# Kernel optimization log

Hardware: AMD Instinct MI355X
Metric: run time of the kernel (lower is better)

Reference implementation:

```python
import jax, jax.numpy as jnp
import numpy as np

MAX_REL_POS = 16  # max_relative_position


def setup_inputs() -> dict:
    key = jax.random.key(0)
    k1, k2, k3 = jax.random.split(key, 3)
    B, H, Lq, Dh = 4, 8, 1024, 64
    L = 1024
    query = jax.random.normal(k1, (B, H, Lq, Dh), dtype=jnp.float32)
    rel_table = jax.random.normal(k2, (2 * MAX_REL_POS + 1, Dh), dtype=jnp.float32)
    time_ids = jnp.sort(jax.random.randint(k3, (B, L), 0, 4096), axis=-1).astype(jnp.int64)
    return {"query": query, "rel_table": rel_table, "time_ids": time_ids, "k_len": 1024}


def reference(query, rel_table, time_ids, k_len):
    # query: (B,H,Lq,Dh), rel_table: (2P+1, Dh), time_ids: (B,L)
    q_len = query.shape[2]
    ts = time_ids[:, :k_len]                       # (B, Lk)
    # relative position: time_k - time_q -> (B, Lq, Lk)
    rel_pos = ts[:, None, :] - ts[:, :q_len, None]
    idx = jnp.clip(rel_pos, -MAX_REL_POS, MAX_REL_POS) + MAX_REL_POS
    rel_emb = rel_table[idx]                       # (B, Lq, Lk, Dh) gather
    # content-to-position scores
    return jnp.einsum("bhqd,bqkd->bhqk", query, rel_emb)
```

## Files before the change

kernel.cpp:

```cpp
#include <hip/hip_runtime.h>

#define MAX_REL 16
#define NTAB    33
#define B       4
#define H       8
#define LQ      1024
#define DH      64
#define KLEN    1024
#define QTILE   16
#define TSTRIDE 68

__global__ __launch_bounds__(256) void fused_pe_kernel(const float* __restrict__ query,
                                                       const float* __restrict__ table,
                                                       const int* __restrict__ time_ids,
                                                       float* __restrict__ out) {
    __shared__ int   ts[KLEN];
    __shared__ float qt[QTILE * DH];
    __shared__ float tb[NTAB * TSTRIDE];
    __shared__ float pr[QTILE * NTAB];

    const int tid  = threadIdx.x;
    const int wave = tid >> 6;
    const int lane = tid & 63;
    const int tile = blockIdx.x;
    const int bh   = tile >> 6;
    const int qt_i = tile & 63;
    const int b    = bh >> 3;
    const int q0   = qt_i * QTILE;
    const int rowbase = bh * LQ + q0;

    ((int4*)ts)[tid] = ((const int4*)(time_ids + b * KLEN))[tid];
    ((float4*)qt)[tid] = ((const float4*)(query + (size_t)rowbase * DH))[tid];
    for (int i = tid; i < NTAB * 16; i += 256) {
        int r = i >> 4, c = i & 15;
        ((float4*)(tb + r * TSTRIDE))[c] = ((const float4*)(table + r * DH))[c];
    }
    __syncthreads();

    const int r0 = wave * 4;
    for (int t = lane; t < 4 * NTAB; t += 64) {
        int r = t / NTAB;
        int j = t - r * NTAB;
        const float4* qv = (const float4*)(qt + (r0 + r) * DH);
        const float4* tv = (const float4*)(tb + j * TSTRIDE);
        float acc = 0.f;
#pragma unroll
        for (int i = 0; i < DH / 4; ++i) {
            float4 a = qv[i];
            float4 w = tv[i];
            acc += a.x * w.x + a.y * w.y + a.z * w.z + a.w * w.w;
        }
        pr[(r0 + r) * NTAB + j] = acc;
    }

    const int4 tk0 = ((const int4*)ts)[0 * 64 + lane];
    const int4 tk1 = ((const int4*)ts)[1 * 64 + lane];
    const int4 tk2 = ((const int4*)ts)[2 * 64 + lane];
    const int4 tk3 = ((const int4*)ts)[3 * 64 + lane];

#pragma unroll
    for (int r = 0; r < 4; ++r) {
        const int row = r0 + r;
        const int tq  = ts[q0 + row];
        const float* prr = pr + row * NTAB;
        float* op = out + (size_t)(rowbase + row) * KLEN + (lane << 2);
#pragma unroll
        for (int c = 0; c < 4; ++c) {
            int4 tk = (c == 0) ? tk0 : (c == 1) ? tk1 : (c == 2) ? tk2 : tk3;
            int i0 = min(max(tk.x - tq, -MAX_REL), MAX_REL) + MAX_REL;
            int i1 = min(max(tk.y - tq, -MAX_REL), MAX_REL) + MAX_REL;
            int i2 = min(max(tk.z - tq, -MAX_REL), MAX_REL) + MAX_REL;
            int i3 = min(max(tk.w - tq, -MAX_REL), MAX_REL) + MAX_REL;
            float4 v = make_float4(prr[i0], prr[i1], prr[i2], prr[i3]);
            *((float4*)(op + c * 256)) = v;
        }
    }
}

extern "C" void kernel_launch(void* const* d_in, const int* in_sizes, int n_in,
                              void* d_out, int out_size, void* d_ws, size_t ws_size,
                              hipStream_t stream) {
    const float* query    = (const float*)d_in[0];
    const float* table    = (const float*)d_in[1];
    const int*   time_ids = (const int*)d_in[2];
    float* out = (float*)d_out;

    fused_pe_kernel<<<B * H * (LQ / QTILE), 256, 0, stream>>>(query, table, time_ids, out);
}
```

Baseline: 146.5 us.

## Compute query-table projection with bf16 MFMA instead of scalar FP32 dot products

Converts the query tile and the relative-position table to bf16 in shared memory, laid out for the matrix cores, and computes the 16x33 projection with mfma_f32_16x16x32_bf16 instructions instead of per-lane FP32 dot products. Each wave computes the full projection redundantly and writes back only its own four rows. This targets the compute phase ahead of the gather/store, but bf16 rounding lowers accuracy. The kernel is likely bound by output writes, so the gain may be small.

```diff
diff --git a/kernel.cpp b/kernel.cpp
--- a/kernel.cpp
+++ b/kernel.cpp
@@ -8,16 +8,25 @@
 #define DH      64
 #define KLEN    1024
 #define QTILE   16
-#define TSTRIDE 68
+#define PRS     48
+
+typedef short s16x8 __attribute__((ext_vector_type(8)));
+typedef float f32x4 __attribute__((ext_vector_type(4)));
+
+static __device__ __forceinline__ short f2bf(float f) {
+    unsigned u = __float_as_uint(f);
+    unsigned r = (u + 0x7FFFu + ((u >> 16) & 1u)) >> 16;
+    return (short)r;
+}
 
 __global__ __launch_bounds__(256) void fused_pe_kernel(const float* __restrict__ query,
                                                        const float* __restrict__ table,
                                                        const int* __restrict__ time_ids,
                                                        float* __restrict__ out) {
     __shared__ int   ts[KLEN];
-    __shared__ float qt[QTILE * DH];
-    __shared__ float tb[NTAB * TSTRIDE];
-    __shared__ float pr[QTILE * NTAB];
+    __shared__ short qth[2 * 64 * 8];
+    __shared__ short tbh[2 * 4 * 48 * 8];
+    __shared__ float pr[QTILE * PRS];
 
     const int tid  = threadIdx.x;
     const int wave = tid >> 6;
@@ -30,27 +39,45 @@
     const int rowbase = bh * LQ + q0;
 
     ((int4*)ts)[tid] = ((const int4*)(time_ids + b * KLEN))[tid];
-    ((float4*)qt)[tid] = ((const float4*)(query + (size_t)rowbase * DH))[tid];
+
+    {
+        float4 v = ((const float4*)(query + (size_t)rowbase * DH))[tid];
+        int m = tid >> 4, c = tid & 15;
+        int kstep = c >> 3, quad = (c >> 1) & 3, jb = (c & 1) << 2;
+        short4 hv = make_short4(f2bf(v.x), f2bf(v.y), f2bf(v.z), f2bf(v.w));
+        *(short4*)(qth + ((kstep * 64 + quad * 16 + m) << 3) + jb) = hv;
+    }
     for (int i = tid; i < NTAB * 16; i += 256) {
-        int r = i >> 4, c = i & 15;
-        ((float4*)(tb + r * TSTRIDE))[c] = ((const float4*)(table + r * DH))[c];
+        int n = i >> 4, c = i & 15;
+        float4 v = ((const float4*)table)[i];
+        int kstep = c >> 3, quad = (c >> 1) & 3, jb = (c & 1) << 2;
+        short4 hv = make_short4(f2bf(v.x), f2bf(v.y), f2bf(v.z), f2bf(v.w));
+        *(short4*)(tbh + (((kstep * 4 + quad) * 48 + n) << 3) + jb) = hv;
     }
     __syncthreads();
 
-    const int r0 = wave * 4;
-    for (int t = lane; t < 4 * NTAB; t += 64) {
-        int r = t / NTAB;
-        int j = t - r * NTAB;
-        const float4* qv = (const float4*)(qt + (r0 + r) * DH);
-        const float4* tv = (const float4*)(tb + j * TSTRIDE);
-        float acc = 0.f;
+    const int quad = lane >> 4;
+    const int nlo  = lane & 15;
+    f32x4 acc0 = {0.f, 0.f, 0.f, 0.f}, acc1 = acc0, acc2 = acc0;
 #pragma unroll
-        for (int i = 0; i < DH / 4; ++i) {
-            float4 a = qv[i];
-            float4 w = tv[i];
-            acc += a.x * w.x + a.y * w.y + a.z * w.z + a.w * w.w;
+    for (int kstep = 0; kstep < 2; ++kstep) {
+        s16x8 a = *(const s16x8*)(qth + ((kstep * 64 + lane) << 3));
+        const short* bbase = tbh + (((kstep * 4 + quad) * 48) << 3);
+        s16x8 b0 = *(const s16x8*)(bbase + (nlo << 3));
+        s16x8 b1 = *(const s16x8*)(bbase + ((nlo + 16) << 3));
+        s16x8 b2 = *(const s16x8*)(bbase + (32 << 3));
+        acc0 = __builtin_amdgcn_mfma_f32_16x16x32_bf16(a, b0, acc0, 0, 0, 0);
+        acc1 = __builtin_amdgcn_mfma_f32_16x16x32_bf16(a, b1, acc1, 0, 0, 0);
+        acc2 = __builtin_amdgcn_mfma_f32_16x16x32_bf16(a, b2, acc2, 0, 0, 0);
+    }
+    if (quad == wave) {
+#pragma unroll
+        for (int i = 0; i < 4; ++i) {
+            int row = wave * 4 + i;
+            pr[row * PRS + nlo]      = acc0[i];
+            pr[row * PRS + 16 + nlo] = acc1[i];
+            pr[row * PRS + 32]       = acc2[i];
         }
-        pr[(r0 + r) * NTAB + j] = acc;
     }
 
     const int4 tk0 = ((const int4*)ts)[0 * 64 + lane];
@@ -60,9 +87,9 @@
 
 #pragma unroll
     for (int r = 0; r < 4; ++r) {
-        const int row = r0 + r;
+        const int row = wave * 4 + r;
         const int tq  = ts[q0 + row];
-        const float* prr = pr + row * NTAB;
+        const float* prr = pr + row * PRS;
         float* op = out + (size_t)(rowbase + row) * KLEN + (lane << 2);
 #pragma unroll
         for (int c = 0; c < 4; ++c) {
```

Result: no change. 143.9 us (-1.8%).
